# Kernel optimization log

Hardware: AMD Instinct MI355X
Metric: run time of the kernel (lower is better)

The kernel has to match this reference:

```python
import jax, jax.numpy as jnp
import numpy as np

E = 1024   # embed_dim
H = 16     # num_heads
D = E // H # head_dim
T = 1024   # tgt_len
S = 1024   # src_len
B = 2      # batch
DELTA = 1.0
SCALE = D ** -0.5


def setup_inputs() -> dict:
    key = jax.random.key(0)
    ks = jax.random.split(key, 16)
    def lin(k, o, i):
        return jax.random.normal(k, (o, i), dtype=jnp.float32) / np.float32(np.sqrt(i))
    return {
        'query': jax.random.normal(ks[0], (T, B, E), dtype=jnp.float32),
        'key_in': jax.random.normal(ks[1], (S, B, E), dtype=jnp.float32),
        'value': jax.random.normal(ks[2], (S, B, E), dtype=jnp.float32),
        'Wq': lin(ks[3], E, E), 'bq': jnp.zeros((E,), jnp.float32),
        'Wk': lin(ks[4], E, E), 'bk': jnp.zeros((E,), jnp.float32),
        'Wv': lin(ks[5], E, E), 'bv': jnp.zeros((E,), jnp.float32),
        'Whq': lin(ks[6], E, E), 'bhq': jnp.zeros((E,), jnp.float32),
        'Whk': lin(ks[7], E, E), 'bhk': jnp.zeros((E,), jnp.float32),
        'Wwp': lin(ks[8], E, E), 'bwp': jnp.zeros((E,), jnp.float32),
        'Wvp': lin(ks[9], 1, E), 'bvp': jnp.zeros((1,), jnp.float32),
        'Wo': lin(ks[10], E, E), 'bo': jnp.zeros((E,), jnp.float32),
    }


def _heads(x, L):
    # (L, B, E) -> (B*H, L, D); E splits as (H, D) so flat index is b*H + h
    return x.reshape(L, B * H, D).transpose(1, 0, 2)


def reference(query, key_in, value, Wq, bq, Wk, bk, Wv, bv, Whq, bhq, Whk, bhk,
              Wwp, bwp, Wvp, bvp, Wo, bo):
    q = (query @ Wq.T + bq) * SCALE
    k = key_in @ Wk.T + bk
    v = value @ Wv.T + bv
    hq = query @ Whq.T + bhq
    hk = key_in @ Whk.T + bhk

    qh, hqh = _heads(q, T), _heads(hq, T)
    kh, hkh, vh = _heads(k, S), _heads(hk, S), _heads(v, S)

    # content attention logits  [B*H, T, S]
    attn = jnp.einsum('btd,bsd->bts', qh, kh)

    # Gaussian center: expected source position from hq/hk alignment
    align = jax.nn.softmax(jnp.einsum('btd,bsd->bts', hqh * SCALE, hkh), axis=-1)
    pos = jnp.arange(S, dtype=attn.dtype)          # index_mask
    mean = align @ pos                              # [B*H, T]

    # Gaussian width: per-query scalar via vp(tanh(wp(query)))
    g = (jnp.tanh(query @ Wwp.T + bwp) @ Wvp.T + bvp)[..., 0]   # (T, B)
    sigma = 1.0 + DELTA * jax.nn.sigmoid(g)                      # (T, B)
    sigma_bh = jnp.broadcast_to(sigma[:, :, None], (T, B, H)).reshape(T, B * H).T

    gauss = -((pos[None, None, :] - mean[:, :, None]) ** 2) / (
        2.0 * sigma_bh[:, :, None] ** 2)

    probs = jax.nn.softmax(attn + gauss, axis=-1)
    out = jnp.einsum('bts,bsd->btd', probs, vh)     # [B*H, T, D]
    out = out.transpose(1, 0, 2).reshape(T, B, E)
    return out @ Wo.T + bo
```

## Files before the change

### kernel.cpp

```cpp
#include <hip/hip_runtime.h>
#include <hip/hip_bf16.h>
#include <hip/hip_fp16.h>

#define T_ 1024
#define S_ 1024
#define B_ 2
#define H_ 16
#define D_ 64
#define E_ 1024
#define M_ (T_*B_)
#define SCALE_ 0.125f
#define LOG2E_ 1.4426950408889634f

typedef __attribute__((ext_vector_type(8))) short short8;
typedef __attribute__((ext_vector_type(8))) _Float16 half8;
typedef __attribute__((ext_vector_type(4))) float f32x4;

#define EXP2 __builtin_amdgcn_exp2f

__device__ __forceinline__ ushort f2bf(float x) {
  unsigned u = __float_as_uint(x);
  unsigned r = (u + 0x7fffu + ((u >> 16) & 1u)) >> 16;
  return (ushort)r;
}
__device__ __forceinline__ float bf2f(ushort h) {
  return __uint_as_float(((unsigned)h) << 16);
}
__device__ __forceinline__ ushort f2h(float x) {
  __half h = __float2half(x);
  return *(ushort*)&h;
}
__device__ __forceinline__ void gld16(const void* g, void* l) {
  __builtin_amdgcn_global_load_lds(
      (const __attribute__((address_space(1))) void*)g,
      (__attribute__((address_space(3))) void*)l, 16, 0, 0);
}
__device__ __forceinline__ unsigned cvtpk_bf16(float a, float b) {
  unsigned u;
  asm("v_cvt_pk_bf16_f32 %0, %1, %2" : "=v"(u) : "v"(a), "v"(b));
  return u;
}

#define SWZ(r, col) ((r)*64 + ((col) ^ (((r)&7)<<3)))

struct CvtDesc { const float* src; ushort* bf; ushort* h16; int n4; };
struct CvtArgs { CvtDesc d[10]; };

__global__ __launch_bounds__(256) void cvt_kernel(CvtArgs a) {
  const CvtDesc d = a.d[blockIdx.y];
  const int stride = gridDim.x * 256;
  for (int i = blockIdx.x*256 + threadIdx.x; i < d.n4; i += stride) {
    float4 v = ((const float4*)d.src)[i];
    float vals[4] = {v.x, v.y, v.z, v.w};
    if (d.bf) {
      ushort h[4];
      #pragma unroll
      for (int j = 0; j < 4; ++j) h[j] = f2bf(vals[j]);
      ((ushort4*)d.bf)[i] = make_ushort4(h[0],h[1],h[2],h[3]);
    }
    if (d.h16) {
      ushort h[4];
      #pragma unroll
      for (int j = 0; j < 4; ++j) h[j] = f2h(vals[j]);
      ((ushort4*)d.h16)[i] = make_ushort4(h[0],h[1],h[2],h[3]);
    }
  }
}

struct SegP { const ushort* A; const ushort* W; const float* bias;
              ushort* outb; float* outf; float scale; int flags; };
struct GemmArgs { SegP s[6]; };

template<int MT>
__global__ __launch_bounds__(256) void gemm_mfma(GemmArgs args) {
  constexpr int AG = MT/32;
  constexpr int MI = MT/32;
  constexpr int NY = 2048/MT;
  __shared__ ushort sA[MT*64];
  __shared__ ushort sW[64*64];
  const int id = blockIdx.x;
  const int xcd = id & 7, loc = id >> 3;
  const int x = xcd * ((gridDim.x >> 3) / NY) + loc / NY;
  const int y = loc % NY;
  const SegP sg = args.s[x >> 4];
  const int n0 = (x & 15) * 64;
  const int m0 = y * MT;
  const int tid = threadIdx.x, wv = tid >> 6, lane = tid & 63;
  const int c = lane & 15, g = lane >> 4;
  const int wr = wv >> 1, wc = wv & 1;
  const int lrow = lane >> 3;
  const int scol = ((lane & 7) ^ lrow) * 8;

  size_t aoff[AG], woff[2];
  #pragma unroll
  for (int j = 0; j < AG; ++j) {
    int rg = wv + j*4;
    aoff[j] = (size_t)(m0 + rg*8 + lrow)*1024 + scol;
  }
  #pragma unroll
  for (int j = 0; j < 2; ++j) {
    int rg = wv + j*4;
    woff[j] = (size_t)(n0 + rg*8 + lrow)*1024 + scol;
  }

  const bool isfp16 = (sg.flags & 2) != 0;
  f32x4 acc[MI][2] = {};
  for (int t = 0; t < 16; ++t) {
    const int k0 = t*64;
    #pragma unroll
    for (int j = 0; j < AG; ++j) {
      int rg = wv + j*4;
      gld16(sg.A + aoff[j] + k0, &sA[rg*512]);
    }
    #pragma unroll
    for (int j = 0; j < 2; ++j) {
      int rg = wv + j*4;
      gld16(sg.W + woff[j] + k0, &sW[rg*512]);
    }
    __syncthreads();
    #pragma unroll
    for (int ks = 0; ks < 2; ++ks) {
      short8 af[MI], wf[2];
      #pragma unroll
      for (int mi = 0; mi < MI; ++mi)
        af[mi] = *(const short8*)&sA[SWZ(wr*(MT/2) + mi*16 + c, ks*32 + g*8)];
      #pragma unroll
      for (int ni = 0; ni < 2; ++ni)
        wf[ni] = *(const short8*)&sW[SWZ(wc*32 + ni*16 + c, ks*32 + g*8)];
      if (isfp16) {
        #pragma unroll
        for (int mi = 0; mi < MI; ++mi)
          #pragma unroll
          for (int ni = 0; ni < 2; ++ni)
            acc[mi][ni] = __builtin_amdgcn_mfma_f32_16x16x32_f16(
                *(half8*)&af[mi], *(half8*)&wf[ni], acc[mi][ni], 0, 0, 0);
      } else {
        #pragma unroll
        for (int mi = 0; mi < MI; ++mi)
          #pragma unroll
          for (int ni = 0; ni < 2; ++ni)
            acc[mi][ni] = __builtin_amdgcn_mfma_f32_16x16x32_bf16(
                af[mi], wf[ni], acc[mi][ni], 0, 0, 0);
      }
    }
    __syncthreads();
  }

  #pragma unroll
  for (int ni = 0; ni < 2; ++ni) {
    int col = n0 + wc*32 + ni*16 + c;
    float bias = sg.bias[col];
    #pragma unroll
    for (int mi = 0; mi < MI; ++mi) {
      #pragma unroll
      for (int r = 0; r < 4; ++r) {
        int row = m0 + wr*(MT/2) + mi*16 + 4*g + r;
        float val = (acc[mi][ni][r] + bias) * sg.scale;
        if (sg.flags & 1) val = tanhf(val);
        if (isfp16)       sg.outb[(size_t)row*1024 + col] = f2h(val);
        else if (sg.outf) sg.outf[(size_t)row*1024 + col] = val;
        else              sg.outb[(size_t)row*1024 + col] = f2bf(val);
      }
    }
  }
}

__global__ __launch_bounds__(64) void vp_sigma(const ushort* __restrict__ wp,
    const float* __restrict__ Wvp, const float* __restrict__ bvp,
    float* __restrict__ sigma) {
  const int m = blockIdx.x;
  const int lane = threadIdx.x;
  float acc = 0.f;
  #pragma unroll
  for (int it = 0; it < 2; ++it) {
    int e = lane*8 + it*512;
    short8 a = *(const short8*)&wp[(size_t)m*E_ + e];
    float4 w0 = *(const float4*)&Wvp[e];
    float4 w1 = *(const float4*)&Wvp[e+4];
    acc += bf2f((ushort)a[0])*w0.x + bf2f((ushort)a[1])*w0.y
         + bf2f((ushort)a[2])*w0.z + bf2f((ushort)a[3])*w0.w
         + bf2f((ushort)a[4])*w1.x + bf2f((ushort)a[5])*w1.y
         + bf2f((ushort)a[6])*w1.z + bf2f((ushort)a[7])*w1.w;
  }
  #pragma unroll
  for (int o = 32; o; o >>= 1) acc += __shfl_xor(acc, o);
  if (lane == 0) {
    float gg = acc + bvp[0];
    sigma[m] = 1.f + 1.f/(1.f + __expf(-gg));
  }
}

__global__ __launch_bounds__(256) void attn_mfma(
    const ushort* __restrict__ q_bf, const ushort* __restrict__ k_bf,
    const ushort* __restrict__ v_bf,
    const ushort* __restrict__ hq_h16, const ushort* __restrict__ hk_h16,
    const float* __restrict__ sigma, ushort* __restrict__ ctx) {
  __shared__ ushort sK[2][64*64];
  __shared__ ushort sV[2][64*64];
  __shared__ ushort sP[4*16*64];

  const int id = blockIdx.x;
  const int loc = id >> 3;
  const int bh = (id & 7) * 4 + (loc >> 4);
  const int b = bh >> 4, h = bh & 15;
  const int t0 = (loc & 15) * 64;
  const int tid = threadIdx.x;
  const int wv = tid >> 6, lane = tid & 63;
  const int c = lane & 15, g = lane >> 4;
  const int qbase = t0 + wv * 16;
  const size_t rowstr = (size_t)B_ * E_;
  const size_t qoff = ((size_t)(qbase + c) * B_ + b) * E_ + h * 64;

  short8 qf[2];
  half8  hqf[2];
  #pragma unroll
  for (int cs = 0; cs < 2; ++cs) {
    qf[cs]  = *(const short8*)&q_bf[qoff + cs*32 + g*8];
    hqf[cs] = *(const half8*)&hq_h16[qoff + cs*32 + g*8];
  }

  const int str0 = wv*16 + (lane >> 3);
  const int str1 = str0 + 8;
  const int chk0 = ((lane & 7) ^ (str0 & 7)) * 8;
  const int chk1 = ((lane & 7) ^ (str1 & 7)) * 8;
  const int ldsst = (wv*16) * 64;

  float den = 0.f, num = 0.f;
  {
    gld16(hk_h16 + ((size_t)str0 * B_ + b) * E_ + h*64 + chk0, &sK[0][ldsst]);
    gld16(hk_h16 + ((size_t)str1 * B_ + b) * E_ + h*64 + chk1, &sK[0][ldsst + 512]);
    __syncthreads();
    for (int t = 0; t < 16; ++t) {
      const ushort* kb = sK[t & 1];
      if (t < 15) {
        int s0n = (t+1) * 64;
        gld16(hk_h16 + ((size_t)(s0n + str0) * B_ + b) * E_ + h*64 + chk0,
              &sK[(t+1) & 1][ldsst]);
        gld16(hk_h16 + ((size_t)(s0n + str1) * B_ + b) * E_ + h*64 + chk1,
              &sK[(t+1) & 1][ldsst + 512]);
      }
      f32x4 acc[4] = {};
      __builtin_amdgcn_s_setprio(1);
      #pragma unroll
      for (int m = 0; m < 4; ++m)
        #pragma unroll
        for (int cs = 0; cs < 2; ++cs)
          acc[m] = __builtin_amdgcn_mfma_f32_16x16x32_f16(
              *(const half8*)&kb[SWZ(c + 16*m, cs*32 + g*8)], hqf[cs], acc[m], 0,0,0);
      __builtin_amdgcn_s_setprio(0);

      float fs = (float)(t*64 + 4*g);
      #pragma unroll
      for (int m = 0; m < 4; ++m)
        #pragma unroll
        for (int r = 0; r < 4; ++r) {
          float e = EXP2(acc[m][r]);
          den += e;
          num += e * (fs + (float)(16*m + r));
        }
      __syncthreads();
    }
  }
  den += __shfl_xor(den, 16); den += __shfl_xor(den, 32);
  num += __shfl_xor(num, 16); num += __shfl_xor(num, 32);
  const float meanq = num / den;
  const float sg = sigma[(size_t)(qbase + c) * B_ + b];
  const float fct = -LOG2E_ / (2.f * sg * sg);

  f32x4 accO[4] = {};
  float denq = 0.f;
  {
    gld16(k_bf + ((size_t)str0 * B_ + b) * E_ + h*64 + chk0, &sK[0][ldsst]);
    gld16(k_bf + ((size_t)str1 * B_ + b) * E_ + h*64 + chk1, &sK[0][ldsst + 512]);
    {
      int s2 = (tid & 31) * 2, d0 = (tid >> 5) * 8;
      size_t off0 = ((size_t)s2 * B_ + b) * E_ + h * 64 + d0;
      uint4 ra = *(const uint4*)&v_bf[off0];
      uint4 rb = *(const uint4*)&v_bf[off0 + rowstr];
      const ushort* pa = (const ushort*)&ra;
      const ushort* pb = (const ushort*)&rb;
      #pragma unroll
      for (int j = 0; j < 8; ++j)
        *(unsigned*)&sV[0][SWZ(d0 + j, s2)] = (unsigned)pa[j] | ((unsigned)pb[j] << 16);
    }
    __syncthreads();

    const int s2v = (tid & 31) * 2, d0v = (tid >> 5) * 8;
    for (int t = 0; t < 16; ++t) {
      const int cur = t & 1;
      const ushort* kb = sK[cur];
      const ushort* vb = sV[cur];
      uint4 ra, rb;
      if (t < 15) {
        int s0n = (t+1) * 64;
        gld16(k_bf + ((size_t)(s0n + str0) * B_ + b) * E_ + h*64 + chk0,
              &sK[cur^1][ldsst]);
        gld16(k_bf + ((size_t)(s0n + str1) * B_ + b) * E_ + h*64 + chk1,
              &sK[cur^1][ldsst + 512]);
        size_t off0 = ((size_t)(s0n + s2v) * B_ + b) * E_ + h * 64 + d0v;
        ra = *(const uint4*)&v_bf[off0];
        rb = *(const uint4*)&v_bf[off0 + rowstr];
      }

      f32x4 accL[4] = {};
      __builtin_amdgcn_s_setprio(1);
      #pragma unroll
      for (int m = 0; m < 4; ++m)
        #pragma unroll
        for (int cs = 0; cs < 2; ++cs)
          accL[m] = __builtin_amdgcn_mfma_f32_16x16x32_bf16(
              *(const short8*)&kb[SWZ(c + 16*m, cs*32 + g*8)], qf[cs], accL[m], 0,0,0);
      __builtin_amdgcn_s_setprio(0);

      float fs = (float)(t*64 + 4*g);
      float psum = 0.f;
      #pragma unroll
      for (int m = 0; m < 4; ++m) {
        float pr[4];
        #pragma unroll
        for (int r = 0; r < 4; ++r) {
          float dd = fs + (float)(16*m + r) - meanq;
          pr[r] = EXP2(accL[m][r] + fct * dd * dd);
          psum += pr[r];
        }
        uint2 uu;
        uu.x = cvtpk_bf16(pr[0], pr[1]);
        uu.y = cvtpk_bf16(pr[2], pr[3]);
        *(uint2*)&sP[wv*1024 + SWZ(c, 16*m + 4*g)] = uu;
      }
      denq += psum;

      __builtin_amdgcn_s_setprio(1);
      #pragma unroll
      for (int n = 0; n < 4; ++n)
        #pragma unroll
        for (int cs = 0; cs < 2; ++cs)
          accO[n] = __builtin_amdgcn_mfma_f32_16x16x32_bf16(
              *(const short8*)&sP[wv*1024 + SWZ(c, cs*32 + 8*g)],
              *(const short8*)&vb[SWZ(c + 16*n, cs*32 + 8*g)],
              accO[n], 0,0,0);
      __builtin_amdgcn_s_setprio(0);

      if (t < 15) {
        const ushort *pa = (const ushort*)&ra, *pb = (const ushort*)&rb;
        #pragma unroll
        for (int j = 0; j < 8; ++j)
          *(unsigned*)&sV[cur^1][SWZ(d0v + j, s2v)] = (unsigned)pa[j] | ((unsigned)pb[j] << 16);
      }
      __syncthreads();
    }
  }

  denq += __shfl_xor(denq, 16);
  denq += __shfl_xor(denq, 32);
  float dinv[4];
  #pragma unroll
  for (int r = 0; r < 4; ++r) dinv[r] = 1.f / __shfl(denq, 4*g + r);

  #pragma unroll
  for (int r = 0; r < 4; ++r) {
    size_t row = ((size_t)(qbase + 4*g + r) * B_ + b) * E_ + h * 64;
    #pragma unroll
    for (int n = 0; n < 4; ++n)
      ctx[row + 16*n + c] = f2bf(accO[n][r] * dinv[r]);
  }
}

extern "C" void kernel_launch(void* const* d_in, const int* in_sizes, int n_in,
                              void* d_out, int out_size, void* d_ws, size_t ws_size,
                              hipStream_t stream) {
  const float* query  = (const float*)d_in[0];
  const float* key_in = (const float*)d_in[1];
  const float* value  = (const float*)d_in[2];
  const float* Wq  = (const float*)d_in[3];  const float* bq  = (const float*)d_in[4];
  const float* Wk  = (const float*)d_in[5];  const float* bk  = (const float*)d_in[6];
  const float* Wv  = (const float*)d_in[7];  const float* bv  = (const float*)d_in[8];
  const float* Whq = (const float*)d_in[9];  const float* bhq = (const float*)d_in[10];
  const float* Whk = (const float*)d_in[11]; const float* bhk = (const float*)d_in[12];
  const float* Wwp = (const float*)d_in[13]; const float* bwp = (const float*)d_in[14];
  const float* Wvp = (const float*)d_in[15]; const float* bvp = (const float*)d_in[16];
  const float* Wo  = (const float*)d_in[17]; const float* bo  = (const float*)d_in[18];

  const size_t AU = (size_t)M_ * E_;
  const size_t WU = (size_t)E_ * E_;
  char* p = (char*)d_ws;
  float*  sig       = (float*)p;  p += 16384;
  ushort* query_bf  = (ushort*)p; p += AU*2;
  ushort* key_bf    = (ushort*)p; p += AU*2;
  ushort* value_bf  = (ushort*)p; p += AU*2;
  ushort* query_h16 = (ushort*)p; p += AU*2;
  ushort* key_h16   = (ushort*)p; p += AU*2;
  ushort* Whq_h16   = (ushort*)p; p += WU*2;
  ushort* Whk_h16   = (ushort*)p; p += WU*2;
  ushort* Wq_bf     = (ushort*)p; p += WU*2;
  ushort* Wk_bf     = (ushort*)p; p += WU*2;
  ushort* Wv_bf     = (ushort*)p; p += WU*2;
  ushort* Wwp_bf    = (ushort*)p; p += WU*2;
  ushort* Wo_bf     = (ushort*)p; p += WU*2;
  ushort* hq_h16    = (ushort*)p; p += AU*2;
  ushort* hk_h16    = (ushort*)p; p += AU*2;
  ushort* q_bf      = (ushort*)p; p += AU*2;
  ushort* k_bf      = (ushort*)p; p += AU*2;
  ushort* v_out     = (ushort*)p; p += AU*2;
  ushort* wp_bf     = (ushort*)p; p += AU*2;
  ushort* ctx_bf    = query_h16;

  {
    CvtArgs a{};
    a.d[0] = {query,  query_bf, query_h16, (int)(AU/4)};
    a.d[1] = {key_in, key_bf,   key_h16,   (int)(AU/4)};
    a.d[2] = {value,  value_bf, nullptr,   (int)(AU/4)};
    a.d[3] = {Whq,    nullptr,  Whq_h16,   (int)(WU/4)};
    a.d[4] = {Whk,    nullptr,  Whk_h16,   (int)(WU/4)};
    a.d[5] = {Wq,     Wq_bf,    nullptr,   (int)(WU/4)};
    a.d[6] = {Wk,     Wk_bf,    nullptr,   (int)(WU/4)};
    a.d[7] = {Wv,     Wv_bf,    nullptr,   (int)(WU/4)};
    a.d[8] = {Wwp,    Wwp_bf,   nullptr,   (int)(WU/4)};
    a.d[9] = {Wo,     Wo_bf,    nullptr,   (int)(WU/4)};
    cvt_kernel<<<dim3(128, 10), 256, 0, stream>>>(a);
  }
  {
    GemmArgs a{};
    a.s[0] = {query_bf,  Wq_bf,   bq,  q_bf,   nullptr, SCALE_*LOG2E_, 0};
    a.s[1] = {query_bf,  Wwp_bf,  bwp, wp_bf,  nullptr, 1.f,           1};
    a.s[2] = {key_bf,    Wk_bf,   bk,  k_bf,   nullptr, 1.f,           0};
    a.s[3] = {value_bf,  Wv_bf,   bv,  v_out,  nullptr, 1.f,           0};
    a.s[4] = {query_h16, Whq_h16, bhq, hq_h16, nullptr, SCALE_*LOG2E_, 2};
    a.s[5] = {key_h16,   Whk_h16, bhk, hk_h16, nullptr, 1.f,           2};
    gemm_mfma<64><<<dim3(3072), 256, 0, stream>>>(a);
  }
  vp_sigma<<<dim3(M_), dim3(64), 0, stream>>>(wp_bf, Wvp, bvp, sig);
  attn_mfma<<<dim3(512), 256, 0, stream>>>(
      q_bf, k_bf, v_out, hq_h16, hk_h16, sig, ctx_bf);
  {
    GemmArgs a{};
    a.s[0] = {ctx_bf, Wo_bf, bo, nullptr, (float*)d_out, 1.f, 0};
    gemm_mfma<64><<<dim3(512), 256, 0, stream>>>(a);
  }
}
```

Measured before the change: 116.8 us.

## Pre-transpose V and read K/V directly from global in single-wave attention blocks

Adds a kernel that transposes V into a per-head [D][S] layout so the P·V MFMA operand can be loaded straight from global memory. The attention kernel changes from 256-thread blocks with double-buffered LDS staging of K and V to 64-thread single-wave blocks that read K, hk and Vt fragments directly from global/L2, keeping LDS only for the P tile. This removes block-wide barriers and LDS traffic and raises block count for occupancy, in exchange for K/V reuse across waves moving from LDS to L2 and an extra transpose launch.

Measured after the change: 170.9 us. 1.46x slower.

```diff
diff --git a/kernel.cpp b/kernel.cpp
--- a/kernel.cpp
+++ b/kernel.cpp
@@ -165,6 +165,33 @@
   }
 }
 
+__global__ __launch_bounds__(256) void vtrans_kernel(
+    const ushort* __restrict__ v, ushort* __restrict__ vt) {
+  __shared__ ushort tile[64][72];
+  const int bh = blockIdx.y;
+  const int b = bh >> 4, h = bh & 15;
+  const int s0 = blockIdx.x * 64;
+  const int tid = threadIdx.x;
+  {
+    int r = tid >> 2;
+    int cch = (tid & 3) * 16;
+    size_t src = ((size_t)(s0 + r) * B_ + b) * E_ + h*64 + cch;
+    *(uint4*)&tile[r][cch]     = *(const uint4*)&v[src];
+    *(uint4*)&tile[r][cch + 8] = *(const uint4*)&v[src + 8];
+  }
+  __syncthreads();
+  {
+    int sl = (tid & 15) * 4;
+    #pragma unroll
+    for (int dp = 0; dp < 4; ++dp) {
+      int d = (tid >> 4) + dp * 16;
+      ushort4 o = make_ushort4(tile[sl+0][d], tile[sl+1][d],
+                               tile[sl+2][d], tile[sl+3][d]);
+      *(ushort4*)&vt[((size_t)(bh*64 + d) << 10) + s0 + sl] = o;
+    }
+  }
+}
+
 __global__ __launch_bounds__(64) void vp_sigma(const ushort* __restrict__ wp,
     const float* __restrict__ Wvp, const float* __restrict__ bvp,
     float* __restrict__ sigma) {
@@ -190,27 +217,22 @@
   }
 }
 
-__global__ __launch_bounds__(256) void attn_mfma(
+__global__ __launch_bounds__(64) void attn_mfma(
     const ushort* __restrict__ q_bf, const ushort* __restrict__ k_bf,
-    const ushort* __restrict__ v_bf,
+    const ushort* __restrict__ vt_bf,
     const ushort* __restrict__ hq_h16, const ushort* __restrict__ hk_h16,
     const float* __restrict__ sigma, ushort* __restrict__ ctx) {
-  __shared__ ushort sK[2][64*64];
-  __shared__ ushort sV[2][64*64];
-  __shared__ ushort sP[4*16*64];
+  __shared__ ushort sP[16*64];
 
   const int id = blockIdx.x;
   const int loc = id >> 3;
-  const int bh = (id & 7) * 4 + (loc >> 4);
+  const int bh = (id & 7) * 4 + (loc >> 6);
   const int b = bh >> 4, h = bh & 15;
-  const int t0 = (loc & 15) * 64;
-  const int tid = threadIdx.x;
-  const int wv = tid >> 6, lane = tid & 63;
+  const int qbase = (loc & 63) * 16;
+  const int lane = threadIdx.x;
   const int c = lane & 15, g = lane >> 4;
-  const int qbase = t0 + wv * 16;
-  const size_t rowstr = (size_t)B_ * E_;
+
   const size_t qoff = ((size_t)(qbase + c) * B_ + b) * E_ + h * 64;
-
   short8 qf[2];
   half8  hqf[2];
   #pragma unroll
@@ -219,47 +241,31 @@
     hqf[cs] = *(const half8*)&hq_h16[qoff + cs*32 + g*8];
   }
 
-  const int str0 = wv*16 + (lane >> 3);
-  const int str1 = str0 + 8;
-  const int chk0 = ((lane & 7) ^ (str0 & 7)) * 8;
-  const int chk1 = ((lane & 7) ^ (str1 & 7)) * 8;
-  const int ldsst = (wv*16) * 64;
+  const size_t kbase = ((size_t)c * B_ + b) * E_ + h*64 + g*8;
+  const size_t mstr = (size_t)16 * B_ * E_;
+  const size_t tstr = (size_t)64 * B_ * E_;
 
   float den = 0.f, num = 0.f;
-  {
-    gld16(hk_h16 + ((size_t)str0 * B_ + b) * E_ + h*64 + chk0, &sK[0][ldsst]);
-    gld16(hk_h16 + ((size_t)str1 * B_ + b) * E_ + h*64 + chk1, &sK[0][ldsst + 512]);
-    __syncthreads();
-    for (int t = 0; t < 16; ++t) {
-      const ushort* kb = sK[t & 1];
-      if (t < 15) {
-        int s0n = (t+1) * 64;
-        gld16(hk_h16 + ((size_t)(s0n + str0) * B_ + b) * E_ + h*64 + chk0,
-              &sK[(t+1) & 1][ldsst]);
-        gld16(hk_h16 + ((size_t)(s0n + str1) * B_ + b) * E_ + h*64 + chk1,
-              &sK[(t+1) & 1][ldsst + 512]);
+  for (int t = 0; t < 16; ++t) {
+    f32x4 acc[4] = {};
+    __builtin_amdgcn_s_setprio(1);
+    #pragma unroll
+    for (int m = 0; m < 4; ++m)
+      #pragma unroll
+      for (int cs = 0; cs < 2; ++cs)
+        acc[m] = __builtin_amdgcn_mfma_f32_16x16x32_f16(
+            *(const half8*)&hk_h16[kbase + (size_t)t*tstr + (size_t)m*mstr + cs*32],
+            hqf[cs], acc[m], 0, 0, 0);
+    __builtin_amdgcn_s_setprio(0);
+    float fs = (float)(t*64 + 4*g);
+    #pragma unroll
+    for (int m = 0; m < 4; ++m)
+      #pragma unroll
+      for (int r = 0; r < 4; ++r) {
+        float e = EXP2(acc[m][r]);
+        den += e;
+        num += e * (fs + (float)(16*m + r));
       }
-      f32x4 acc[4] = {};
-      __builtin_amdgcn_s_setprio(1);
-      #pragma unroll
-      for (int m = 0; m < 4; ++m)
-        #pragma unroll
-        for (int cs = 0; cs < 2; ++cs)
-          acc[m] = __builtin_amdgcn_mfma_f32_16x16x32_f16(
-              *(const half8*)&kb[SWZ(c + 16*m, cs*32 + g*8)], hqf[cs], acc[m], 0,0,0);
-      __builtin_amdgcn_s_setprio(0);
-
-      float fs = (float)(t*64 + 4*g);
-      #pragma unroll
-      for (int m = 0; m < 4; ++m)
-        #pragma unroll
-        for (int r = 0; r < 4; ++r) {
-          float e = EXP2(acc[m][r]);
-          den += e;
-          num += e * (fs + (float)(16*m + r));
-        }
-      __syncthreads();
-    }
   }
   den += __shfl_xor(den, 16); den += __shfl_xor(den, 32);
   num += __shfl_xor(num, 16); num += __shfl_xor(num, 32);
@@ -269,86 +275,51 @@
 
   f32x4 accO[4] = {};
   float denq = 0.f;
-  {
-    gld16(k_bf + ((size_t)str0 * B_ + b) * E_ + h*64 + chk0, &sK[0][ldsst]);
-    gld16(k_bf + ((size_t)str1 * B_ + b) * E_ + h*64 + chk1, &sK[0][ldsst + 512]);
-    {
-      int s2 = (tid & 31) * 2, d0 = (tid >> 5) * 8;
-      size_t off0 = ((size_t)s2 * B_ + b) * E_ + h * 64 + d0;
-      uint4 ra = *(const uint4*)&v_bf[off0];
-      uint4 rb = *(const uint4*)&v_bf[off0 + rowstr];
-      const ushort* pa = (const ushort*)&ra;
-      const ushort* pb = (const ushort*)&rb;
-      #pragma unroll
-      for (int j = 0; j < 8; ++j)
-        *(unsigned*)&sV[0][SWZ(d0 + j, s2)] = (unsigned)pa[j] | ((unsigned)pb[j] << 16);
-    }
-    __syncthreads();
-
-    const int s2v = (tid & 31) * 2, d0v = (tid >> 5) * 8;
-    for (int t = 0; t < 16; ++t) {
-      const int cur = t & 1;
-      const ushort* kb = sK[cur];
-      const ushort* vb = sV[cur];
-      uint4 ra, rb;
-      if (t < 15) {
-        int s0n = (t+1) * 64;
-        gld16(k_bf + ((size_t)(s0n + str0) * B_ + b) * E_ + h*64 + chk0,
-              &sK[cur^1][ldsst]);
-        gld16(k_bf + ((size_t)(s0n + str1) * B_ + b) * E_ + h*64 + chk1,
-              &sK[cur^1][ldsst + 512]);
-        size_t off0 = ((size_t)(s0n + s2v) * B_ + b) * E_ + h * 64 + d0v;
-        ra = *(const uint4*)&v_bf[off0];
-        rb = *(const uint4*)&v_bf[off0 + rowstr];
+  const size_t vbase = ((size_t)(bh*64 + c) << 10) + g*8;
+  for (int t = 0; t < 16; ++t) {
+    f32x4 accL[4] = {};
+    __builtin_amdgcn_s_setprio(1);
+    #pragma unroll
+    for (int m = 0; m < 4; ++m)
+      #pragma unroll
+      for (int cs = 0; cs < 2; ++cs)
+        accL[m] = __builtin_amdgcn_mfma_f32_16x16x32_bf16(
+            *(const short8*)&k_bf[kbase + (size_t)t*tstr + (size_t)m*mstr + cs*32],
+            qf[cs], accL[m], 0, 0, 0);
+    __builtin_amdgcn_s_setprio(0);
+
+    float fs = (float)(t*64 + 4*g);
+    float psum = 0.f;
+    #pragma unroll
+    for (int m = 0; m < 4; ++m) {
+      float pr[4];
+      #pragma unroll
+      for (int r = 0; r < 4; ++r) {
+        float dd = fs + (float)(16*m + r) - meanq;
+        pr[r] = EXP2(accL[m][r] + fct * dd * dd);
+        psum += pr[r];
       }
-
-      f32x4 accL[4] = {};
-      __builtin_amdgcn_s_setprio(1);
-      #pragma unroll
-      for (int m = 0; m < 4; ++m)
-        #pragma unroll
-        for (int cs = 0; cs < 2; ++cs)
-          accL[m] = __builtin_amdgcn_mfma_f32_16x16x32_bf16(
-              *(const short8*)&kb[SWZ(c + 16*m, cs*32 + g*8)], qf[cs], accL[m], 0,0,0);
-      __builtin_amdgcn_s_setprio(0);
-
-      float fs = (float)(t*64 + 4*g);
-      float psum = 0.f;
-      #pragma unroll
-      for (int m = 0; m < 4; ++m) {
-        float pr[4];
-        #pragma unroll
-        for (int r = 0; r < 4; ++r) {
-          float dd = fs + (float)(16*m + r) - meanq;
-          pr[r] = EXP2(accL[m][r] + fct * dd * dd);
-          psum += pr[r];
-        }
-        uint2 uu;
-        uu.x = cvtpk_bf16(pr[0], pr[1]);
-        uu.y = cvtpk_bf16(pr[2], pr[3]);
-        *(uint2*)&sP[wv*1024 + SWZ(c, 16*m + 4*g)] = uu;
-      }
-      denq += psum;
-
-      __builtin_amdgcn_s_setprio(1);
-      #pragma unroll
-      for (int n = 0; n < 4; ++n)
-        #pragma unroll
-        for (int cs = 0; cs < 2; ++cs)
-          accO[n] = __builtin_amdgcn_mfma_f32_16x16x32_bf16(
-              *(const short8*)&sP[wv*1024 + SWZ(c, cs*32 + 8*g)],
-              *(const short8*)&vb[SWZ(c + 16*n, cs*32 + 8*g)],
-              accO[n], 0,0,0);
-      __builtin_amdgcn_s_setprio(0);
-
-      if (t < 15) {
-        const ushort *pa = (const ushort*)&ra, *pb = (const ushort*)&rb;
-        #pragma unroll
-        for (int j = 0; j < 8; ++j)
-          *(unsigned*)&sV[cur^1][SWZ(d0v + j, s2v)] = (unsigned)pa[j] | ((unsigned)pb[j] << 16);
-      }
-      __syncthreads();
-    }
+      uint2 uu;
+      uu.x = cvtpk_bf16(pr[0], pr[1]);
+      uu.y = cvtpk_bf16(pr[2], pr[3]);
+      *(uint2*)&sP[SWZ(c, 16*m + 4*g)] = uu;
+    }
+    denq += psum;
+
+    short8 pf[2];
+    #pragma unroll
+    for (int cs = 0; cs < 2; ++cs)
+      pf[cs] = *(const short8*)&sP[SWZ(c, cs*32 + 8*g)];
+    __builtin_amdgcn_s_setprio(1);
+    #pragma unroll
+    for (int n = 0; n < 4; ++n)
+      #pragma unroll
+      for (int cs = 0; cs < 2; ++cs)
+        accO[n] = __builtin_amdgcn_mfma_f32_16x16x32_bf16(
+            pf[cs],
+            *(const short8*)&vt_bf[vbase + (size_t)(n*16 << 10) + t*64 + cs*32],
+            accO[n], 0, 0, 0);
+    __builtin_amdgcn_s_setprio(0);
   }
 
   denq += __shfl_xor(denq, 16);
@@ -404,6 +375,7 @@
   ushort* v_out     = (ushort*)p; p += AU*2;
   ushort* wp_bf     = (ushort*)p; p += AU*2;
   ushort* ctx_bf    = query_h16;
+  ushort* vt_bf     = key_h16;
 
   {
     CvtArgs a{};
@@ -429,9 +401,10 @@
     a.s[5] = {key_h16,   Whk_h16, bhk, hk_h16, nullptr, 1.f,           2};
     gemm_mfma<64><<<dim3(3072), 256, 0, stream>>>(a);
   }
+  vtrans_kernel<<<dim3(16, 32), 256, 0, stream>>>(v_out, vt_bf);
   vp_sigma<<<dim3(M_), dim3(64), 0, stream>>>(wp_bf, Wvp, bvp, sig);
-  attn_mfma<<<dim3(512), 256, 0, stream>>>(
-      q_bf, k_bf, v_out, hq_h16, hk_h16, sig, ctx_bf);
+  attn_mfma<<<dim3(2048), 64, 0, stream>>>(
+      q_bf, k_bf, vt_bf, hq_h16, hk_h16, sig, ctx_bf);
   {
     GemmArgs a{};
     a.s[0] = {ctx_bf, Wo_bf, bo, nullptr, (float*)d_out, 1.f, 0};
```

## Split attention blocks into 32-query tiles with two waves per block

Applied to the files above, without the earlier changes.

Reworks the attention kernel to use 128-thread blocks (two waves) covering 32 query rows each, doubling the grid to 1024 blocks. K/V staging loops are restructured so each thread loads four rows of K and four rows of V per tile instead of two. The aim is more blocks for better CU occupancy and load balance across the GPU, at the cost of loading each K/V tile twice as often per query, which raises global and LDS traffic.

New measurement: 120.8 us. 1.03x slower.

```diff
diff --git a/kernel.cpp b/kernel.cpp
--- a/kernel.cpp
+++ b/kernel.cpp
@@ -190,20 +190,20 @@
   }
 }
 
-__global__ __launch_bounds__(256) void attn_mfma(
+__global__ __launch_bounds__(128) void attn_mfma(
     const ushort* __restrict__ q_bf, const ushort* __restrict__ k_bf,
     const ushort* __restrict__ v_bf,
     const ushort* __restrict__ hq_h16, const ushort* __restrict__ hk_h16,
     const float* __restrict__ sigma, ushort* __restrict__ ctx) {
   __shared__ ushort sK[2][64*64];
   __shared__ ushort sV[2][64*64];
-  __shared__ ushort sP[4*16*64];
+  __shared__ ushort sP[2][16*64];
 
   const int id = blockIdx.x;
   const int loc = id >> 3;
-  const int bh = (id & 7) * 4 + (loc >> 4);
+  const int bh = (id & 7) * 4 + (loc >> 5);
   const int b = bh >> 4, h = bh & 15;
-  const int t0 = (loc & 15) * 64;
+  const int t0 = (loc & 31) * 32;
   const int tid = threadIdx.x;
   const int wv = tid >> 6, lane = tid & 63;
   const int c = lane & 15, g = lane >> 4;
@@ -219,26 +219,30 @@
     hqf[cs] = *(const half8*)&hq_h16[qoff + cs*32 + g*8];
   }
 
-  const int str0 = wv*16 + (lane >> 3);
-  const int str1 = str0 + 8;
-  const int chk0 = ((lane & 7) ^ (str0 & 7)) * 8;
-  const int chk1 = ((lane & 7) ^ (str1 & 7)) * 8;
-  const int ldsst = (wv*16) * 64;
+  const int lrow = lane >> 3;
+  const int chk = ((lane & 7) ^ lrow) * 8;
+  size_t kgoff[4];
+  #pragma unroll
+  for (int j = 0; j < 4; ++j) {
+    int row = wv*32 + j*8 + lrow;
+    kgoff[j] = ((size_t)row * B_ + b) * E_ + h*64 + chk;
+  }
+  #define KSTAGE(dst, src, soff)                                      \
+    _Pragma("unroll")                                                 \
+    for (int j = 0; j < 4; ++j)                                       \
+      gld16((src) + kgoff[j] + (size_t)(soff) * rowstr,               \
+            &(dst)[(wv*32 + j*8)*64]);
+
+  const int s2v = (tid & 15) * 4;
+  const int d0v = (tid >> 4) * 8;
 
   float den = 0.f, num = 0.f;
   {
-    gld16(hk_h16 + ((size_t)str0 * B_ + b) * E_ + h*64 + chk0, &sK[0][ldsst]);
-    gld16(hk_h16 + ((size_t)str1 * B_ + b) * E_ + h*64 + chk1, &sK[0][ldsst + 512]);
+    KSTAGE(sK[0], hk_h16, 0);
     __syncthreads();
     for (int t = 0; t < 16; ++t) {
       const ushort* kb = sK[t & 1];
-      if (t < 15) {
-        int s0n = (t+1) * 64;
-        gld16(hk_h16 + ((size_t)(s0n + str0) * B_ + b) * E_ + h*64 + chk0,
-              &sK[(t+1) & 1][ldsst]);
-        gld16(hk_h16 + ((size_t)(s0n + str1) * B_ + b) * E_ + h*64 + chk1,
-              &sK[(t+1) & 1][ldsst + 512]);
-      }
+      if (t < 15) { KSTAGE(sK[(t+1) & 1], hk_h16, (t+1)*64); }
       f32x4 acc[4] = {};
       __builtin_amdgcn_s_setprio(1);
       #pragma unroll
@@ -270,36 +274,35 @@
   f32x4 accO[4] = {};
   float denq = 0.f;
   {
-    gld16(k_bf + ((size_t)str0 * B_ + b) * E_ + h*64 + chk0, &sK[0][ldsst]);
-    gld16(k_bf + ((size_t)str1 * B_ + b) * E_ + h*64 + chk1, &sK[0][ldsst + 512]);
+    KSTAGE(sK[0], k_bf, 0);
     {
-      int s2 = (tid & 31) * 2, d0 = (tid >> 5) * 8;
-      size_t off0 = ((size_t)s2 * B_ + b) * E_ + h * 64 + d0;
-      uint4 ra = *(const uint4*)&v_bf[off0];
-      uint4 rb = *(const uint4*)&v_bf[off0 + rowstr];
-      const ushort* pa = (const ushort*)&ra;
-      const ushort* pb = (const ushort*)&rb;
-      #pragma unroll
-      for (int j = 0; j < 8; ++j)
-        *(unsigned*)&sV[0][SWZ(d0 + j, s2)] = (unsigned)pa[j] | ((unsigned)pb[j] << 16);
+      size_t off0 = ((size_t)s2v * B_ + b) * E_ + h * 64 + d0v;
+      uint4 r0 = *(const uint4*)&v_bf[off0];
+      uint4 r1 = *(const uint4*)&v_bf[off0 + rowstr];
+      uint4 r2 = *(const uint4*)&v_bf[off0 + 2*rowstr];
+      uint4 r3 = *(const uint4*)&v_bf[off0 + 3*rowstr];
+      const ushort *p0 = (const ushort*)&r0, *p1 = (const ushort*)&r1;
+      const ushort *p2 = (const ushort*)&r2, *p3 = (const ushort*)&r3;
+      #pragma unroll
+      for (int j = 0; j < 8; ++j) {
+        *(unsigned*)&sV[0][SWZ(d0v + j, s2v)]     = (unsigned)p0[j] | ((unsigned)p1[j] << 16);
+        *(unsigned*)&sV[0][SWZ(d0v + j, s2v + 2)] = (unsigned)p2[j] | ((unsigned)p3[j] << 16);
+      }
     }
     __syncthreads();
 
-    const int s2v = (tid & 31) * 2, d0v = (tid >> 5) * 8;
     for (int t = 0; t < 16; ++t) {
       const int cur = t & 1;
       const ushort* kb = sK[cur];
       const ushort* vb = sV[cur];
-      uint4 ra, rb;
+      uint4 r0, r1, r2, r3;
       if (t < 15) {
-        int s0n = (t+1) * 64;
-        gld16(k_bf + ((size_t)(s0n + str0) * B_ + b) * E_ + h*64 + chk0,
-              &sK[cur^1][ldsst]);
-        gld16(k_bf + ((size_t)(s0n + str1) * B_ + b) * E_ + h*64 + chk1,
-              &sK[cur^1][ldsst + 512]);
-        size_t off0 = ((size_t)(s0n + s2v) * B_ + b) * E_ + h * 64 + d0v;
-        ra = *(const uint4*)&v_bf[off0];
-        rb = *(const uint4*)&v_bf[off0 + rowstr];
+        KSTAGE(sK[cur^1], k_bf, (t+1)*64);
+        size_t off0 = ((size_t)((t+1)*64 + s2v) * B_ + b) * E_ + h * 64 + d0v;
+        r0 = *(const uint4*)&v_bf[off0];
+        r1 = *(const uint4*)&v_bf[off0 + rowstr];
+        r2 = *(const uint4*)&v_bf[off0 + 2*rowstr];
+        r3 = *(const uint4*)&v_bf[off0 + 3*rowstr];
       }
 
       f32x4 accL[4] = {};
@@ -326,7 +329,7 @@
         uint2 uu;
         uu.x = cvtpk_bf16(pr[0], pr[1]);
         uu.y = cvtpk_bf16(pr[2], pr[3]);
-        *(uint2*)&sP[wv*1024 + SWZ(c, 16*m + 4*g)] = uu;
+        *(uint2*)&sP[wv][SWZ(c, 16*m + 4*g)] = uu;
       }
       denq += psum;
 
@@ -336,20 +339,24 @@
         #pragma unroll
         for (int cs = 0; cs < 2; ++cs)
           accO[n] = __builtin_amdgcn_mfma_f32_16x16x32_bf16(
-              *(const short8*)&sP[wv*1024 + SWZ(c, cs*32 + 8*g)],
+              *(const short8*)&sP[wv][SWZ(c, cs*32 + 8*g)],
               *(const short8*)&vb[SWZ(c + 16*n, cs*32 + 8*g)],
               accO[n], 0,0,0);
       __builtin_amdgcn_s_setprio(0);
 
       if (t < 15) {
-        const ushort *pa = (const ushort*)&ra, *pb = (const ushort*)&rb;
-        #pragma unroll
-        for (int j = 0; j < 8; ++j)
-          *(unsigned*)&sV[cur^1][SWZ(d0v + j, s2v)] = (unsigned)pa[j] | ((unsigned)pb[j] << 16);
+        const ushort *p0 = (const ushort*)&r0, *p1 = (const ushort*)&r1;
+        const ushort *p2 = (const ushort*)&r2, *p3 = (const ushort*)&r3;
+        #pragma unroll
+        for (int j = 0; j < 8; ++j) {
+          *(unsigned*)&sV[cur^1][SWZ(d0v + j, s2v)]     = (unsigned)p0[j] | ((unsigned)p1[j] << 16);
+          *(unsigned*)&sV[cur^1][SWZ(d0v + j, s2v + 2)] = (unsigned)p2[j] | ((unsigned)p3[j] << 16);
+        }
       }
       __syncthreads();
     }
   }
+  #undef KSTAGE
 
   denq += __shfl_xor(denq, 16);
   denq += __shfl_xor(denq, 32);
@@ -430,7 +437,7 @@
     gemm_mfma<64><<<dim3(3072), 256, 0, stream>>>(a);
   }
   vp_sigma<<<dim3(M_), dim3(64), 0, stream>>>(wp_bf, Wvp, bvp, sig);
-  attn_mfma<<<dim3(512), 256, 0, stream>>>(
+  attn_mfma<<<dim3(1024), 128, 0, stream>>>(
       q_bf, k_bf, v_out, hq_h16, hk_h16, sig, ctx_bf);
   {
     GemmArgs a{};
```
